# Kernel tuning notes

Measured on AMD Instinct MI355X. Metric: run time of the kernel, lower is better.

Reference implementation:

```python
import jax, jax.numpy as jnp
import numpy as np

GRID_NUM = 3  # pykan 'grid' (number of intervals)
K = 3         # spline order

def bspline_basis(x, grid, k):
    # Cox-de Boor recursion, matching pykan B_batch with a shared extended grid.
    # x: (N, Din); grid: (G,) extended grid with G = GRID_NUM + 2*k + 1
    x = x[..., None]  # (N, Din, 1)
    B = ((x >= grid[:-1]) & (x < grid[1:])).astype(x.dtype)  # (N, Din, G-1)
    for p in range(1, k + 1):
        left = (x - grid[:-(p + 1)]) / (grid[p:-1] - grid[:-(p + 1)])
        right = (grid[p + 1:] - x) / (grid[p + 1:] - grid[1:-p])
        B = left * B[..., :-1] + right * B[..., 1:]
    return B  # (N, Din, GRID_NUM + k)

def setup_inputs() -> dict:
    key = jax.random.key(0)
    k1, k2, k3 = jax.random.split(key, 3)
    Bsz, S, Din, Dout = 4, 2048, 768, 768
    x = jax.random.normal(k1, (Bsz, S, Din), dtype=jnp.float32)
    # noise-scale-like init for spline coefficients (noise_scale=0.1)
    coef = (0.1 / GRID_NUM) * jax.random.normal(k2, (Dout, Din, GRID_NUM + K), dtype=jnp.float32)
    inv_sqrt_in = np.float32(1.0 / np.sqrt(Din))
    scale_base = inv_sqrt_in + 0.1 * inv_sqrt_in * jax.random.normal(k3, (Dout, Din), dtype=jnp.float32)
    scale_sp = jnp.ones((Dout, Din), dtype=jnp.float32)
    bias = jnp.zeros((Dout,), dtype=jnp.float32)
    return {"x": x, "coef": coef, "scale_base": scale_base, "scale_sp": scale_sp, "bias": bias}

def reference(x, coef, scale_base, scale_sp, bias):
    # x: (B, S, Din) -> flatten tokens as the original module does
    Bsz, S, Din = x.shape
    xf = x.reshape(-1, Din)  # (N, Din)
    # extended grid: linspace(-1,1,GRID_NUM+1) extended by K points each side (h = 2/GRID_NUM)
    h = 2.0 / GRID_NUM
    grid = jnp.arange(-K, GRID_NUM + K + 1, dtype=x.dtype) * h - 1.0  # (GRID_NUM + 2K + 1,)
    basis = bspline_basis(xf, grid, K)  # (N, Din, GRID_NUM+K)
    # per-edge activation: scale_base*silu(x) + scale_sp*spline(x); mask==1; symbolic branch==0
    base = jax.nn.silu(xf) @ scale_base.T  # (N, Dout)
    spline = jnp.einsum('nim,oim->no', basis, scale_sp[:, :, None] * coef)  # (N, Dout)
    out = base + spline + bias  # bias from pykan biases[l].weight
    return out.reshape(Bsz, S, -1)
```

## Files before the change

### kernel.cpp

```cpp
#include <hip/hip_runtime.h>
#include <hip/hip_bf16.h>


typedef _Float16 f16;
typedef __attribute__((ext_vector_type(8))) _Float16 f16x8;
typedef __attribute__((ext_vector_type(4))) float f32x4;

#define NTOK 8192
#define DIN 768
#define DOUT 768
#define KAUG 5376
#define BM 128
#define BN 128
#define BK 32
#define KSPLIT 2
#define KSEG (KAUG / KSPLIT)
#define KT (KSEG / BK)

typedef __attribute__((address_space(1))) void gvoid;
typedef __attribute__((address_space(3))) void lvoid;

__global__ __launch_bounds__(256) void build_A(const float* __restrict__ x,
                                               f16* __restrict__ Aa) {
  const int t = blockIdx.x * 256 + threadIdx.x;
  const int n = t / 96;
  const int i8 = (t - n * 96) * 8;

  const float4* xp = (const float4*)(x + (size_t)n * DIN + i8);
  float4 va = xp[0], vb = xp[1];
  float xv[8] = {va.x, va.y, va.z, va.w, vb.x, vb.y, vb.z, vb.w};

  f16x8 sil;
  f16x8 Bv[6];
#pragma unroll
  for (int e = 0; e < 8; ++e) {
    const float v = xv[e];
    sil[e] = (f16)__fdividef(v, 1.0f + __expf(-v));

    const float s = (v + 1.0f) * 1.5f + 3.0f;
    const float fi = floorf(s);
    const int i0 = (int)fi;
    const float u = s - fi;
    const float um = 1.0f - u;
    const float u2 = u * u, u3 = u2 * u;
    const float w0 = um * um * um * (1.0f / 6.0f);
    const float w1 = (3.0f * u3 - 6.0f * u2 + 4.0f) * (1.0f / 6.0f);
    const float w2 = (-3.0f * u3 + 3.0f * u2 + 3.0f * u + 1.0f) * (1.0f / 6.0f);
    const float w3 = u3 * (1.0f / 6.0f);
#pragma unroll
    for (int m = 0; m < 6; ++m) {
      const int d = m - i0 + 3;
      float w = (d == 0) ? w0 : (d == 1) ? w1 : (d == 2) ? w2 : (d == 3) ? w3 : 0.0f;
      Bv[m][e] = (f16)w;
    }
  }

  const size_t base = (size_t)n * KAUG + i8;
  *(f16x8*)&Aa[base] = sil;
#pragma unroll
  for (int m = 0; m < 6; ++m) *(f16x8*)&Aa[base + (size_t)(m + 1) * DIN] = Bv[m];
}

__global__ __launch_bounds__(256) void build_W(const float* __restrict__ sb,
                                               const float* __restrict__ ssp,
                                               const float* __restrict__ coef,
                                               f16* __restrict__ Wa) {
  int idx = blockIdx.x * 256 + threadIdx.x;
  float b = sb[idx];
  float sp = ssp[idx];
  int o = idx / DIN;
  int i = idx - o * DIN;
  size_t base = (size_t)o * KAUG + i;
  Wa[base] = (f16)b;
#pragma unroll
  for (int m = 0; m < 6; ++m)
    Wa[base + (size_t)(m + 1) * DIN] = (f16)(sp * coef[(size_t)idx * 6 + m]);
}

__global__ __launch_bounds__(256, 3) void kan_gemm(const f16* __restrict__ A,
                                                   const f16* __restrict__ W,
                                                   const float* __restrict__ bias,
                                                   float* __restrict__ out) {
  __shared__ alignas(16) f16 As[2][BM * BK];
  __shared__ alignas(16) f16 Bs[2][BN * BK];

  const int bid = blockIdx.x;
  const int xcd = bid & 7;
  const int slot = bid >> 3;
  const int mb = ((slot & 7) << 3) + xcd;
  const int rest = slot >> 3;
  const int nb = rest % 6;
  const int ks = rest / 6;
  const int m0 = mb * BM;
  const int n0 = nb * BN;
  const size_t kbase = (size_t)ks * KSEG;

  const int tid = threadIdx.x;
  const int wave = tid >> 6;
  const int lane = tid & 63;
  const int wm = (wave >> 1) * 64;
  const int wn = (wave & 1) * 64;
  const int r = lane & 15;
  const int q = lane >> 4;

  f32x4 acc[4][4] = {};

  const int c0 = wave * 64 + lane;
  const int rowA0 = c0 >> 2, kb0 = c0 & 3;
  const int c1 = c0 + 256;
  const int rowA1 = c1 >> 2, kb1 = c1 & 3;

  const f16* gA0 = A + (size_t)(m0 + rowA0) * KAUG + kbase + kb0 * 8;
  const f16* gA1 = A + (size_t)(m0 + rowA1) * KAUG + kbase + kb1 * 8;
  const f16* gB0 = W + (size_t)(n0 + rowA0) * KAUG + kbase + kb0 * 8;
  const f16* gB1 = W + (size_t)(n0 + rowA1) * KAUG + kbase + kb1 * 8;

  const int woff = wave * 512;

  auto stage = [&](int buf, int kt) {
    const int koff = kt * BK;
    __builtin_amdgcn_global_load_lds((gvoid*)(gA0 + koff), (lvoid*)(&As[buf][woff]), 16, 0, 0);
    __builtin_amdgcn_global_load_lds((gvoid*)(gA1 + koff), (lvoid*)(&As[buf][woff + 2048]), 16, 0, 0);
    __builtin_amdgcn_global_load_lds((gvoid*)(gB0 + koff), (lvoid*)(&Bs[buf][woff]), 16, 0, 0);
    __builtin_amdgcn_global_load_lds((gvoid*)(gB1 + koff), (lvoid*)(&Bs[buf][woff + 2048]), 16, 0, 0);
  };

  stage(0, 0);

  for (int kt = 0; kt < KT; ++kt) {
    const int buf = kt & 1;
    __syncthreads();
    if (kt + 1 < KT) stage(buf ^ 1, kt + 1);

    f16x8 af[4], bf[4];
#pragma unroll
    for (int mi = 0; mi < 4; ++mi)
      af[mi] = *(const f16x8*)&As[buf][(wm + mi * 16 + r) * BK + q * 8];
#pragma unroll
    for (int ni = 0; ni < 4; ++ni)
      bf[ni] = *(const f16x8*)&Bs[buf][(wn + ni * 16 + r) * BK + q * 8];
#pragma unroll
    for (int mi = 0; mi < 4; ++mi)
#pragma unroll
      for (int ni = 0; ni < 4; ++ni)
        acc[mi][ni] =
            __builtin_amdgcn_mfma_f32_16x16x32_f16(af[mi], bf[ni], acc[mi][ni], 0, 0, 0);
  }

#pragma unroll
  for (int ni = 0; ni < 4; ++ni) {
    const int gcol = n0 + wn + ni * 16 + r;
    const float badd = (ks == 0) ? bias[gcol] : 0.0f;
#pragma unroll
    for (int mi = 0; mi < 4; ++mi) {
#pragma unroll
      for (int rg = 0; rg < 4; ++rg) {
        const int grow = m0 + wm + mi * 16 + q * 4 + rg;
        atomicAdd(&out[(size_t)grow * DOUT + gcol], acc[mi][ni][rg] + badd);
      }
    }
  }
}

extern "C" void kernel_launch(void* const* d_in, const int* in_sizes, int n_in,
                              void* d_out, int out_size, void* d_ws, size_t ws_size,
                              hipStream_t stream) {
  const float* x = (const float*)d_in[0];
  const float* coef = (const float*)d_in[1];
  const float* scale_base = (const float*)d_in[2];
  const float* scale_sp = (const float*)d_in[3];
  const float* bias = (const float*)d_in[4];
  float* out = (float*)d_out;

  f16* Aa = (f16*)d_ws;
  f16* Wa = (f16*)((char*)d_ws + (size_t)NTOK * KAUG * 2);

  hipMemsetAsync(d_out, 0, (size_t)out_size * sizeof(float), stream);

  build_A<<<(NTOK * DIN / 8) / 256, 256, 0, stream>>>(x, Aa);
  build_W<<<(DOUT * DIN) / 256, 256, 0, stream>>>(scale_base, scale_sp, coef, Wa);
  kan_gemm<<<KSPLIT * 6 * 64, 256, 0, stream>>>(Aa, Wa, bias, out);
}
```

Measured before the change: 227.5 us.

## Retile GEMM to 96-wide N tiles and fuse prep kernels with output zeroing

Changes the GEMM N tile from 128 to 96 so the grid becomes 1024 blocks at four blocks per CU, aiming for a more even fill of the compute units. It merges build_A, a vectorized build_W and the output zeroing into one launch, removing the memset and extra launch overhead. The cost is a lower MFMA-to-load ratio per wave, and some waves idle during B-tile staging.

```diff
diff --git a/kernel.cpp b/kernel.cpp
--- a/kernel.cpp
+++ b/kernel.cpp
@@ -11,73 +11,101 @@
 #define DOUT 768
 #define KAUG 5376
 #define BM 128
-#define BN 128
+#define BN 96
 #define BK 32
 #define KSPLIT 2
 #define KSEG (KAUG / KSPLIT)
 #define KT (KSEG / BK)
 
+#define A_BLOCKS 3072
+#define W_BLOCKS 288
+#define Z_BLOCKS 1536
+
 typedef __attribute__((address_space(1))) void gvoid;
 typedef __attribute__((address_space(3))) void lvoid;
 
-__global__ __launch_bounds__(256) void build_A(const float* __restrict__ x,
-                                               f16* __restrict__ Aa) {
-  const int t = blockIdx.x * 256 + threadIdx.x;
-  const int n = t / 96;
-  const int i8 = (t - n * 96) * 8;
-
-  const float4* xp = (const float4*)(x + (size_t)n * DIN + i8);
-  float4 va = xp[0], vb = xp[1];
-  float xv[8] = {va.x, va.y, va.z, va.w, vb.x, vb.y, vb.z, vb.w};
-
-  f16x8 sil;
-  f16x8 Bv[6];
-#pragma unroll
-  for (int e = 0; e < 8; ++e) {
-    const float v = xv[e];
-    sil[e] = (f16)__fdividef(v, 1.0f + __expf(-v));
-
-    const float s = (v + 1.0f) * 1.5f + 3.0f;
-    const float fi = floorf(s);
-    const int i0 = (int)fi;
-    const float u = s - fi;
-    const float um = 1.0f - u;
-    const float u2 = u * u, u3 = u2 * u;
-    const float w0 = um * um * um * (1.0f / 6.0f);
-    const float w1 = (3.0f * u3 - 6.0f * u2 + 4.0f) * (1.0f / 6.0f);
-    const float w2 = (-3.0f * u3 + 3.0f * u2 + 3.0f * u + 1.0f) * (1.0f / 6.0f);
-    const float w3 = u3 * (1.0f / 6.0f);
-#pragma unroll
-    for (int m = 0; m < 6; ++m) {
-      const int d = m - i0 + 3;
-      float w = (d == 0) ? w0 : (d == 1) ? w1 : (d == 2) ? w2 : (d == 3) ? w3 : 0.0f;
-      Bv[m][e] = (f16)w;
+__global__ __launch_bounds__(256) void build_all(const float* __restrict__ x,
+                                                 const float* __restrict__ sb,
+                                                 const float* __restrict__ ssp,
+                                                 const float* __restrict__ coef,
+                                                 f16* __restrict__ Aa,
+                                                 f16* __restrict__ Wa,
+                                                 float* __restrict__ out) {
+  const int b = blockIdx.x;
+  if (b < A_BLOCKS) {
+    const int t = b * 256 + threadIdx.x;
+    const int n = t / 96;
+    const int i8 = (t - n * 96) * 8;
+
+    const float4* xp = (const float4*)(x + (size_t)n * DIN + i8);
+    float4 va = xp[0], vb = xp[1];
+    float xv[8] = {va.x, va.y, va.z, va.w, vb.x, vb.y, vb.z, vb.w};
+
+    f16x8 sil;
+    f16x8 Bv[6];
+#pragma unroll
+    for (int e = 0; e < 8; ++e) {
+      const float v = xv[e];
+      sil[e] = (f16)__fdividef(v, 1.0f + __expf(-v));
+
+      const float s = (v + 1.0f) * 1.5f + 3.0f;
+      const float fi = floorf(s);
+      const int i0 = (int)fi;
+      const float u = s - fi;
+      const float um = 1.0f - u;
+      const float u2 = u * u, u3 = u2 * u;
+      const float w0 = um * um * um * (1.0f / 6.0f);
+      const float w1 = (3.0f * u3 - 6.0f * u2 + 4.0f) * (1.0f / 6.0f);
+      const float w2 = (-3.0f * u3 + 3.0f * u2 + 3.0f * u + 1.0f) * (1.0f / 6.0f);
+      const float w3 = u3 * (1.0f / 6.0f);
+#pragma unroll
+      for (int m = 0; m < 6; ++m) {
+        const int d = m - i0 + 3;
+        float w = (d == 0) ? w0 : (d == 1) ? w1 : (d == 2) ? w2 : (d == 3) ? w3 : 0.0f;
+        Bv[m][e] = (f16)w;
+      }
     }
+
+    const size_t base = (size_t)n * KAUG + i8;
+    *(f16x8*)&Aa[base] = sil;
+#pragma unroll
+    for (int m = 0; m < 6; ++m) *(f16x8*)&Aa[base + (size_t)(m + 1) * DIN] = Bv[m];
+  } else if (b < A_BLOCKS + W_BLOCKS) {
+    const int t = (b - A_BLOCKS) * 256 + threadIdx.x;
+    const int o = t / 96;
+    const int i8 = (t - o * 96) * 8;
+    const size_t idx = (size_t)o * DIN + i8;
+
+    float bb[8], sp[8], cf[48];
+    *(float4*)&bb[0] = ((const float4*)(sb + idx))[0];
+    *(float4*)&bb[4] = ((const float4*)(sb + idx))[1];
+    *(float4*)&sp[0] = ((const float4*)(ssp + idx))[0];
+    *(float4*)&sp[4] = ((const float4*)(ssp + idx))[1];
+#pragma unroll
+    for (int v = 0; v < 12; ++v) *(float4*)&cf[v * 4] = ((const float4*)(coef + idx * 6))[v];
+
+    f16x8 ch0;
+    f16x8 chm[6];
+#pragma unroll
+    for (int e = 0; e < 8; ++e) {
+      ch0[e] = (f16)bb[e];
+#pragma unroll
+      for (int m = 0; m < 6; ++m) chm[m][e] = (f16)(sp[e] * cf[e * 6 + m]);
+    }
+    const size_t base = (size_t)o * KAUG + i8;
+    *(f16x8*)&Wa[base] = ch0;
+#pragma unroll
+    for (int m = 0; m < 6; ++m) *(f16x8*)&Wa[base + (size_t)(m + 1) * DIN] = chm[m];
+  } else {
+    const int t = (b - A_BLOCKS - W_BLOCKS) * 256 + threadIdx.x;
+    float4* o4 = (float4*)out;
+    const float4 z = {0.f, 0.f, 0.f, 0.f};
+#pragma unroll
+    for (int s = 0; s < 4; ++s) o4[(size_t)t * 4 + s] = z;
   }
-
-  const size_t base = (size_t)n * KAUG + i8;
-  *(f16x8*)&Aa[base] = sil;
-#pragma unroll
-  for (int m = 0; m < 6; ++m) *(f16x8*)&Aa[base + (size_t)(m + 1) * DIN] = Bv[m];
 }
 
-__global__ __launch_bounds__(256) void build_W(const float* __restrict__ sb,
-                                               const float* __restrict__ ssp,
-                                               const float* __restrict__ coef,
-                                               f16* __restrict__ Wa) {
-  int idx = blockIdx.x * 256 + threadIdx.x;
-  float b = sb[idx];
-  float sp = ssp[idx];
-  int o = idx / DIN;
-  int i = idx - o * DIN;
-  size_t base = (size_t)o * KAUG + i;
-  Wa[base] = (f16)b;
-#pragma unroll
-  for (int m = 0; m < 6; ++m)
-    Wa[base + (size_t)(m + 1) * DIN] = (f16)(sp * coef[(size_t)idx * 6 + m]);
-}
-
-__global__ __launch_bounds__(256, 3) void kan_gemm(const f16* __restrict__ A,
+__global__ __launch_bounds__(256, 4) void kan_gemm(const f16* __restrict__ A,
                                                    const f16* __restrict__ W,
                                                    const float* __restrict__ bias,
                                                    float* __restrict__ out) {
@@ -89,8 +117,8 @@
   const int slot = bid >> 3;
   const int mb = ((slot & 7) << 3) + xcd;
   const int rest = slot >> 3;
-  const int nb = rest % 6;
-  const int ks = rest / 6;
+  const int nb = rest & 7;
+  const int ks = rest >> 3;
   const int m0 = mb * BM;
   const int n0 = nb * BN;
   const size_t kbase = (size_t)ks * KSEG;
@@ -99,21 +127,21 @@
   const int wave = tid >> 6;
   const int lane = tid & 63;
   const int wm = (wave >> 1) * 64;
-  const int wn = (wave & 1) * 64;
+  const int wn = (wave & 1) * 48;
   const int r = lane & 15;
   const int q = lane >> 4;
 
-  f32x4 acc[4][4] = {};
+  f32x4 acc[4][3] = {};
 
   const int c0 = wave * 64 + lane;
-  const int rowA0 = c0 >> 2, kb0 = c0 & 3;
+  const int rowA0 = c0 >> 2, kq0 = c0 & 3;
   const int c1 = c0 + 256;
-  const int rowA1 = c1 >> 2, kb1 = c1 & 3;
-
-  const f16* gA0 = A + (size_t)(m0 + rowA0) * KAUG + kbase + kb0 * 8;
-  const f16* gA1 = A + (size_t)(m0 + rowA1) * KAUG + kbase + kb1 * 8;
-  const f16* gB0 = W + (size_t)(n0 + rowA0) * KAUG + kbase + kb0 * 8;
-  const f16* gB1 = W + (size_t)(n0 + rowA1) * KAUG + kbase + kb1 * 8;
+  const int rowA1 = c1 >> 2, kq1 = c1 & 3;
+
+  const f16* gA0 = A + (size_t)(m0 + rowA0) * KAUG + kbase + kq0 * 8;
+  const f16* gA1 = A + (size_t)(m0 + rowA1) * KAUG + kbase + kq1 * 8;
+  const f16* gB0 = W + (size_t)(n0 + rowA0) * KAUG + kbase + kq0 * 8;
+  const f16* gB1 = W + (size_t)(n0 + rowA1) * KAUG + kbase + kq1 * 8;
 
   const int woff = wave * 512;
 
@@ -122,7 +150,8 @@
     __builtin_amdgcn_global_load_lds((gvoid*)(gA0 + koff), (lvoid*)(&As[buf][woff]), 16, 0, 0);
     __builtin_amdgcn_global_load_lds((gvoid*)(gA1 + koff), (lvoid*)(&As[buf][woff + 2048]), 16, 0, 0);
     __builtin_amdgcn_global_load_lds((gvoid*)(gB0 + koff), (lvoid*)(&Bs[buf][woff]), 16, 0, 0);
-    __builtin_amdgcn_global_load_lds((gvoid*)(gB1 + koff), (lvoid*)(&Bs[buf][woff + 2048]), 16, 0, 0);
+    if (wave < 2)
+      __builtin_amdgcn_global_load_lds((gvoid*)(gB1 + koff), (lvoid*)(&Bs[buf][woff + 2048]), 16, 0, 0);
   };
 
   stage(0, 0);
@@ -132,23 +161,23 @@
     __syncthreads();
     if (kt + 1 < KT) stage(buf ^ 1, kt + 1);
 
-    f16x8 af[4], bf[4];
+    f16x8 af[4], bf[3];
 #pragma unroll
     for (int mi = 0; mi < 4; ++mi)
       af[mi] = *(const f16x8*)&As[buf][(wm + mi * 16 + r) * BK + q * 8];
 #pragma unroll
-    for (int ni = 0; ni < 4; ++ni)
+    for (int ni = 0; ni < 3; ++ni)
       bf[ni] = *(const f16x8*)&Bs[buf][(wn + ni * 16 + r) * BK + q * 8];
 #pragma unroll
     for (int mi = 0; mi < 4; ++mi)
 #pragma unroll
-      for (int ni = 0; ni < 4; ++ni)
+      for (int ni = 0; ni < 3; ++ni)
         acc[mi][ni] =
             __builtin_amdgcn_mfma_f32_16x16x32_f16(af[mi], bf[ni], acc[mi][ni], 0, 0, 0);
   }
 
 #pragma unroll
-  for (int ni = 0; ni < 4; ++ni) {
+  for (int ni = 0; ni < 3; ++ni) {
     const int gcol = n0 + wn + ni * 16 + r;
     const float badd = (ks == 0) ? bias[gcol] : 0.0f;
 #pragma unroll
@@ -175,9 +204,7 @@
   f16* Aa = (f16*)d_ws;
   f16* Wa = (f16*)((char*)d_ws + (size_t)NTOK * KAUG * 2);
 
-  hipMemsetAsync(d_out, 0, (size_t)out_size * sizeof(float), stream);
-
-  build_A<<<(NTOK * DIN / 8) / 256, 256, 0, stream>>>(x, Aa);
-  build_W<<<(DOUT * DIN) / 256, 256, 0, stream>>>(scale_base, scale_sp, coef, Wa);
-  kan_gemm<<<KSPLIT * 6 * 64, 256, 0, stream>>>(Aa, Wa, bias, out);
+  build_all<<<A_BLOCKS + W_BLOCKS + Z_BLOCKS, 256, 0, stream>>>(x, scale_base, scale_sp,
+                                                                coef, Aa, Wa, out);
+  kan_gemm<<<8 * 128, 256, 0, stream>>>(Aa, Wa, bias, out);
 }
```

Result: no change. 228.6 us (+0.5%).
